# Kernel optimization log

Hardware: AMD Instinct MI355X
Metric: run time of the kernel (lower is better)

Reference implementation:

```python
import jax, jax.numpy as jnp
import numpy as np

TAU = 0.5  # threshold from init kwargs
INF = jnp.float32(1e30)


def setup_inputs() -> dict:
    key = jax.random.key(0)
    k1, k2 = jax.random.split(key)
    B, H, W = 16, 96, 96
    prediction = jax.random.uniform(k1, (B, H, W), dtype=jnp.float32)
    target = jax.random.uniform(k2, (B, H, W), dtype=jnp.float32)
    return {"prediction": prediction, "target": target}


def _grid_dist(H, W):
    # Euclidean distances between all (row, col) pixel coordinates -> [N, N]
    yy, xx = jnp.meshgrid(jnp.arange(H), jnp.arange(W), indexing="ij")
    coords = jnp.stack([yy.ravel(), xx.ravel()], axis=-1).astype(jnp.float32)  # [N, 2]
    sq = jnp.sum(coords * coords, axis=-1)  # [N]
    d2 = sq[:, None] + sq[None, :] - 2.0 * (coords @ coords.T)
    return jnp.sqrt(jnp.maximum(d2, 0.0))


def reference(prediction, target):
    B, H, W = prediction.shape
    N = H * W
    D = _grid_dist(H, W)  # shared across the batch: coord set is the full grid

    pred = (prediction >= TAU).reshape(B, N)   # bool masks selecting grid points
    label = (target >= TAU).reshape(B, N)

    def per_image(masks):
        a, b = masks  # bool [N], bool [N]
        any_a = jnp.any(a)
        any_b = jnp.any(b)
        # directed distances: for each point in one set, min dist to other set
        min_ab = jnp.min(jnp.where(b[None, :], D, INF), axis=1)   # [N]
        d_ab = jnp.max(jnp.where(a, min_ab, -INF))                # max over set A
        min_ba = jnp.min(jnp.where(a[:, None], D, INF), axis=0)   # [N]
        d_ba = jnp.max(jnp.where(b, min_ba, -INF))
        hd_both = jnp.maximum(d_ab, d_ba)
        # empty-set rules: one empty -> diameter of the other; both empty -> 0
        diam_a = jnp.max(jnp.where(a[:, None] & a[None, :], D, -INF))
        diam_b = jnp.max(jnp.where(b[:, None] & b[None, :], D, -INF))
        return jnp.where(
            any_a & any_b,
            hd_both,
            jnp.where(any_a, diam_a, jnp.where(any_b, diam_b, jnp.float32(0.0))),
        )

    # sequential over batch to keep peak memory at one [N, N] masked buffer
    hd = jax.lax.map(per_image, (pred, label))  # [B]
    return jnp.mean(hd)  # reduction == 'mean'
```

## Files before the change

### kernel.cpp

```cpp
#include <hip/hip_runtime.h>
#include <limits.h>

#define HB 16
#define HH 96
#define HW 96
#define HN (HH*HW)
#define WPR 3
#define WPI (HH*WPR)
#define TPB 1024
#define PXT (HN/TPB)

__device__ __forceinline__ int nearest_dx(unsigned long long lo, unsigned int hi, int x) {
    int dr = 1 << 20, dl = 1 << 20;
    if (x < 64) {
        unsigned long long r = lo >> x;
        if (r) dr = __builtin_ctzll(r);
        else if (hi) dr = (64 - x) + __builtin_ctz(hi);
        unsigned long long lm = lo << (63 - x);
        if (lm) dl = __builtin_clzll(lm);
    } else {
        int xh = x - 64;
        unsigned int r = hi >> xh;
        if (r) dr = __builtin_ctz(r);
        unsigned int lmh = hi << (31 - xh);
        if (lmh) dl = __builtin_clz(lmh);
        else if (lo) dl = (xh + 1) + __builtin_clzll(lo);
    }
    return min(dl, dr);
}

__device__ __forceinline__ int farthest_dx(unsigned long long lo, unsigned int hi, int x) {
    int first = lo ? __builtin_ctzll(lo) : 64 + __builtin_ctz(hi);
    int last  = hi ? 95 - __builtin_clz(hi) : 63 - __builtin_clzll(lo);
    return max(x - first, last - x);
}

__device__ __forceinline__ int search2d(const unsigned int* m, int y, int x) {
    int best = INT_MAX;
    for (int dy = 0; dy < HH; ++dy) {
        if (dy * dy >= best) break;
        int yl = y - dy;
        if (yl >= 0) {
            unsigned long long lo = (unsigned long long)m[yl*WPR] |
                                    ((unsigned long long)m[yl*WPR+1] << 32);
            unsigned int hi = m[yl*WPR+2];
            if (lo | hi) {
                int dx = nearest_dx(lo, hi, x);
                best = min(best, dy*dy + dx*dx);
            }
        }
        int yh = y + dy;
        if (dy > 0 && yh < HH) {
            unsigned long long lo = (unsigned long long)m[yh*WPR] |
                                    ((unsigned long long)m[yh*WPR+1] << 32);
            unsigned int hi = m[yh*WPR+2];
            if (lo | hi) {
                int dx = nearest_dx(lo, hi, x);
                best = min(best, dy*dy + dx*dx);
            }
        }
    }
    return best;
}

__device__ __forceinline__ int farthest2d(const unsigned int* m, int y, int x) {
    int best = 0;
    for (int yy = 0; yy < HH; ++yy) {
        unsigned long long lo = (unsigned long long)m[yy*WPR] |
                                ((unsigned long long)m[yy*WPR+1] << 32);
        unsigned int hi = m[yy*WPR+2];
        if (lo | hi) {
            int fd = farthest_dx(lo, hi, x);
            int dy = yy - y;
            best = max(best, dy*dy + fd*fd);
        }
    }
    return best;
}

__global__ __launch_bounds__(TPB) void hausdorff_fused(const float* __restrict__ pred,
                                                       const float* __restrict__ targ,
                                                       float* __restrict__ out) {
    int img = blockIdx.x;
    int tid = threadIdx.x;
    __shared__ unsigned int sA[WPI], sB[WPI];
    __shared__ int redAB, redBA;
    __shared__ int fA, fB;

    if (tid == 0) { redAB = -1; redBA = -1; fA = 0; fB = 0; }

    if (tid < 2 * WPI) {
        int set = tid >= WPI;
        int w   = set ? tid - WPI : tid;
        const float* src = (set ? targ : pred) + img * HN + 32 * w;
        const float4* v4 = reinterpret_cast<const float4*>(src);
        unsigned int bits = 0;
        #pragma unroll
        for (int j = 0; j < 8; ++j) {
            float4 v = v4[j];
            if (v.x >= 0.5f) bits |= 1u << (4*j + 0);
            if (v.y >= 0.5f) bits |= 1u << (4*j + 1);
            if (v.z >= 0.5f) bits |= 1u << (4*j + 2);
            if (v.w >= 0.5f) bits |= 1u << (4*j + 3);
        }
        (set ? sB : sA)[w] = bits;
        if (bits) { if (set) fB = 1; else fA = 1; }
    }
    __syncthreads();

    bool anyA = fA != 0, anyB = fB != 0;
    int lAB = -1, lBA = -1;

    if (anyA && anyB) {
        #pragma unroll
        for (int k = 0; k < PXT; ++k) {
            int li = k * TPB + tid;
            int y  = li / HW;
            int x  = li - y * HW;
            bool a = (sA[y*WPR + (x>>5)] >> (x & 31)) & 1u;
            bool b = (sB[y*WPR + (x>>5)] >> (x & 31)) & 1u;
            if (a) lAB = max(lAB, search2d(sB, y, x));
            if (b) lBA = max(lBA, search2d(sA, y, x));
        }
    } else if (anyA) {
        for (int k = 0; k < PXT; ++k) {
            int li = k * TPB + tid;
            int y  = li / HW;
            int x  = li - y * HW;
            bool a = (sA[y*WPR + (x>>5)] >> (x & 31)) & 1u;
            if (a) lAB = max(lAB, farthest2d(sA, y, x));
        }
    } else if (anyB) {
        for (int k = 0; k < PXT; ++k) {
            int li = k * TPB + tid;
            int y  = li / HW;
            int x  = li - y * HW;
            bool b = (sB[y*WPR + (x>>5)] >> (x & 31)) & 1u;
            if (b) lBA = max(lBA, farthest2d(sB, y, x));
        }
    }

    #pragma unroll
    for (int off = 32; off >= 1; off >>= 1) {
        lAB = max(lAB, __shfl_down(lAB, off, 64));
        lBA = max(lBA, __shfl_down(lBA, off, 64));
    }
    if ((tid & 63) == 0) {
        atomicMax(&redAB, lAB);
        atomicMax(&redBA, lBA);
    }
    __syncthreads();

    if (tid == 0) {
        float hd;
        if (anyA && anyB)      hd = sqrtf((float)max(redAB, redBA));
        else if (anyA)         hd = sqrtf((float)redAB);
        else if (anyB)         hd = sqrtf((float)redBA);
        else                   hd = 0.0f;
        atomicAdd(out, hd * (1.0f / HB));
    }
}

extern "C" void kernel_launch(void* const* d_in, const int* in_sizes, int n_in,
                              void* d_out, int out_size, void* d_ws, size_t ws_size,
                              hipStream_t stream) {
    const float* pred = (const float*)d_in[0];
    const float* targ = (const float*)d_in[1];
    float* out = (float*)d_out;

    hipMemsetAsync(out, 0, sizeof(float), stream);
    hausdorff_fused<<<HB, TPB, 0, stream>>>(pred, targ, out);
}
```

Measured before the change: 76.85 us.

## Split each image into row stripes across many blocks with last-block reduction

Instead of one 1024-thread block per image (16 blocks total), each image is split into 12 row stripes handled by 256-thread blocks, giving 192 blocks to fill more compute units. Each block still rebuilds the full image bitmasks in shared memory, then publishes per-image maxima through global atomics, and the last block to finish computes the mean. The intent is to cut the per-block serial search latency. The cost is redundant bitmask loads per stripe plus a global counter and threadfence handoff. The workspace is memset to 0xFF, so the counter starts at -1, which is why the last block checks NBLK-2.

```diff
diff --git a/kernel.cpp b/kernel.cpp
--- a/kernel.cpp
+++ b/kernel.cpp
@@ -7,8 +7,11 @@
 #define HN (HH*HW)
 #define WPR 3
 #define WPI (HH*WPR)
-#define TPB 1024
-#define PXT (HN/TPB)
+#define STRIPES 12
+#define ROWS_PER (HH/STRIPES)
+#define PX_PER (ROWS_PER*HW)
+#define TPB 256
+#define NBLK (HB*STRIPES)
 
 __device__ __forceinline__ int nearest_dx(unsigned long long lo, unsigned int hi, int x) {
     int dr = 1 << 20, dl = 1 << 20;
@@ -44,10 +47,8 @@
             unsigned long long lo = (unsigned long long)m[yl*WPR] |
                                     ((unsigned long long)m[yl*WPR+1] << 32);
             unsigned int hi = m[yl*WPR+2];
-            if (lo | hi) {
-                int dx = nearest_dx(lo, hi, x);
-                best = min(best, dy*dy + dx*dx);
-            }
+            if (lo | hi) best = min(best, dy*dy + [&]{
+                int dx = nearest_dx(lo, hi, x); return dx*dx; }());
         }
         int yh = y + dy;
         if (dy > 0 && yh < HH) {
@@ -80,19 +81,24 @@
 
 __global__ __launch_bounds__(TPB) void hausdorff_fused(const float* __restrict__ pred,
                                                        const float* __restrict__ targ,
+                                                       int* __restrict__ gAB,
+                                                       int* __restrict__ gBA,
+                                                       int* __restrict__ cnt,
                                                        float* __restrict__ out) {
-    int img = blockIdx.x;
-    int tid = threadIdx.x;
+    int blk    = blockIdx.x;
+    int img    = blk / STRIPES;
+    int stripe = blk - img * STRIPES;
+    int tid    = threadIdx.x;
+
     __shared__ unsigned int sA[WPI], sB[WPI];
-    __shared__ int redAB, redBA;
-    __shared__ int fA, fB;
-
+    __shared__ int redAB, redBA, fA, fB, isLast;
     if (tid == 0) { redAB = -1; redBA = -1; fA = 0; fB = 0; }
-
-    if (tid < 2 * WPI) {
-        int set = tid >= WPI;
-        int w   = set ? tid - WPI : tid;
-        const float* src = (set ? targ : pred) + img * HN + 32 * w;
+    __syncthreads();
+
+    for (int w = tid; w < 2 * WPI; w += TPB) {
+        int set = w >= WPI;
+        int ww  = set ? w - WPI : w;
+        const float* src = (set ? targ : pred) + img * HN + 32 * ww;
         const float4* v4 = reinterpret_cast<const float4*>(src);
         unsigned int bits = 0;
         #pragma unroll
@@ -103,40 +109,43 @@
             if (v.z >= 0.5f) bits |= 1u << (4*j + 2);
             if (v.w >= 0.5f) bits |= 1u << (4*j + 3);
         }
-        (set ? sB : sA)[w] = bits;
+        (set ? sB : sA)[ww] = bits;
         if (bits) { if (set) fB = 1; else fA = 1; }
     }
     __syncthreads();
 
     bool anyA = fA != 0, anyB = fB != 0;
     int lAB = -1, lBA = -1;
+    int y0 = stripe * ROWS_PER;
 
     if (anyA && anyB) {
-        #pragma unroll
-        for (int k = 0; k < PXT; ++k) {
-            int li = k * TPB + tid;
-            int y  = li / HW;
-            int x  = li - y * HW;
+        for (int k = 0; k < PX_PER; k += TPB) {
+            int li = k + tid;
+            int ry = li / HW;
+            int y  = y0 + ry;
+            int x  = li - ry * HW;
             bool a = (sA[y*WPR + (x>>5)] >> (x & 31)) & 1u;
             bool b = (sB[y*WPR + (x>>5)] >> (x & 31)) & 1u;
             if (a) lAB = max(lAB, search2d(sB, y, x));
             if (b) lBA = max(lBA, search2d(sA, y, x));
         }
     } else if (anyA) {
-        for (int k = 0; k < PXT; ++k) {
-            int li = k * TPB + tid;
-            int y  = li / HW;
-            int x  = li - y * HW;
-            bool a = (sA[y*WPR + (x>>5)] >> (x & 31)) & 1u;
-            if (a) lAB = max(lAB, farthest2d(sA, y, x));
+        for (int k = 0; k < PX_PER; k += TPB) {
+            int li = k + tid;
+            int ry = li / HW;
+            int y  = y0 + ry;
+            int x  = li - ry * HW;
+            if ((sA[y*WPR + (x>>5)] >> (x & 31)) & 1u)
+                lAB = max(lAB, farthest2d(sA, y, x));
         }
     } else if (anyB) {
-        for (int k = 0; k < PXT; ++k) {
-            int li = k * TPB + tid;
-            int y  = li / HW;
-            int x  = li - y * HW;
-            bool b = (sB[y*WPR + (x>>5)] >> (x & 31)) & 1u;
-            if (b) lBA = max(lBA, farthest2d(sB, y, x));
+        for (int k = 0; k < PX_PER; k += TPB) {
+            int li = k + tid;
+            int ry = li / HW;
+            int y  = y0 + ry;
+            int x  = li - ry * HW;
+            if ((sB[y*WPR + (x>>5)] >> (x & 31)) & 1u)
+                lBA = max(lBA, farthest2d(sB, y, x));
         }
     }
 
@@ -152,12 +161,27 @@
     __syncthreads();
 
     if (tid == 0) {
-        float hd;
-        if (anyA && anyB)      hd = sqrtf((float)max(redAB, redBA));
-        else if (anyA)         hd = sqrtf((float)redAB);
-        else if (anyB)         hd = sqrtf((float)redBA);
-        else                   hd = 0.0f;
-        atomicAdd(out, hd * (1.0f / HB));
+        atomicMax(&gAB[img], redAB);
+        atomicMax(&gBA[img], redBA);
+        __threadfence();
+        int old = atomicAdd(cnt, 1);
+        isLast = (old == NBLK - 2);
+    }
+    __syncthreads();
+
+    if (isLast) {
+        float hd = 0.0f;
+        if (tid < HB) {
+            int vAB = atomicMax(&gAB[tid], INT_MIN);
+            int vBA = atomicMax(&gBA[tid], INT_MIN);
+            hd = sqrtf((float)max(max(vAB, vBA), 0));
+        }
+        if (tid < 64) {
+            #pragma unroll
+            for (int off = 8; off >= 1; off >>= 1)
+                hd += __shfl_down(hd, off, 16);
+            if (tid == 0) out[0] = hd * (1.0f / HB);
+        }
     }
 }
 
@@ -168,6 +192,10 @@
     const float* targ = (const float*)d_in[1];
     float* out = (float*)d_out;
 
-    hipMemsetAsync(out, 0, sizeof(float), stream);
-    hausdorff_fused<<<HB, TPB, 0, stream>>>(pred, targ, out);
-}
+    int* gAB = (int*)d_ws;
+    int* gBA = gAB + HB;
+    int* cnt = gBA + HB;
+    hipMemsetAsync(d_ws, 0xFF, (2 * HB + 1) * sizeof(int), stream);
+
+    hausdorff_fused<<<NBLK, TPB, 0, stream>>>(pred, targ, gAB, gBA, cnt, out);
+}
```

After: 69.79 us. 9.2% less time.
